# Optimization experiments

Hardware: AMD Instinct MI355X
Metric: run time of the kernel (lower is better)

The kernel has to match this reference:

```python
import jax, jax.numpy as jnp
import numpy as np

P, Q, R = 3, 1, 0          # CliffordAlgebra(p=3, q=1, r=0)
N = P + Q + R
ALG = 1 << N               # 16 basis blades
SHIFTS = (1, 2, 4)


def _cayley():
    """Cayley table C[i,j,k]: blade_i * blade_j = C[i,j,i^j] * blade_{i^j}."""
    metric = [1.0] * P + [-1.0] * Q + [0.0] * R
    C = np.zeros((ALG, ALG, ALG), np.float32)
    for a in range(ALG):
        for b in range(ALG):
            x = a >> 1
            s = 0
            while x:                       # reordering sign
                s += bin(x & b).count('1')
                x >>= 1
            val = -1.0 if (s & 1) else 1.0
            for i in range(N):             # metric for repeated basis vectors
                if (a & b) >> i & 1:
                    val *= metric[i]
            C[a, b, a ^ b] = val
    return C

_C = _cayley()
C0 = jnp.asarray(_C[:, :, 0])                        # grade-0 slice: <a*b>_0
A = jnp.asarray((_C - _C.transpose(1, 0, 2)) / 2.0)  # antisym: (ab - ba)/2
VEC_MASK = jnp.asarray(np.array([1.0 if bin(i).count('1') == 1 else 0.0 for i in range(ALG)], np.float32))
BIV_MASK = jnp.asarray(np.array([1.0 if bin(i).count('1') == 2 else 0.0 for i in range(ALG)], np.float32))


def setup_inputs() -> dict:
    key = jax.random.key(0)
    k1, k2 = jax.random.split(key, 2)
    B, T, D = 8, 4096, 1024
    return {
        "x": jax.random.normal(k1, (B, T, D), jnp.float32),
        "gate_w": jax.random.normal(k2, (D, 1), jnp.float32) * 0.02,
        "gate_b": jnp.zeros((1,), jnp.float32),
        "scalar_weight": jnp.float32(0.5),
        "bivector_weight": jnp.float32(0.5),
    }


def reference(x, gate_w, gate_b, scalar_weight, bivector_weight):
    B, T, D = x.shape
    n = D // ALG                         # 64 chunks of 16 (D divisible, no pad)
    ss = jax.nn.sigmoid(scalar_weight)
    sb = jax.nn.sigmoid(bivector_weight)
    gate = jax.nn.sigmoid(x @ gate_w + gate_b)   # (B,T,1), gate of x (loop-invariant)
    xc = x.reshape(B, T, n, ALG)
    out = x
    for shift in SHIFTS:                 # T=4096 > shift always
        c = x - jnp.roll(x, shift, axis=1)
        cc = c.reshape(B, T, n, ALG)
        # inner product: scalar part per chunk, summed over chunks
        scalar = jnp.einsum('btni,btnj,ij->bt', xc, cc, C0)
        # wedge: antisymmetrized geometric product of vector-grade projections
        av = xc * VEC_MASK
        bv = cc * VEC_MASK
        wedge = jnp.einsum('btni,btnj,ijk->btnk', av, bv, A) * BIV_MASK
        delta = (sb * wedge).reshape(B, T, D)
        delta = delta.at[..., 0].add(ss * scalar)   # scalar_part lives at index 0
        out = out + gate * delta
    return out
```

## Files before the change

kernel.cpp:

```cpp
#include <hip/hip_runtime.h>
#include <math.h>


constexpr int T_DIM = 4096;
constexpr int D_DIM = 1024;
constexpr int ROWS_PER_BLOCK = 4;

__device__ __forceinline__ float sigmoidf(float z) {
    return 1.0f / (1.0f + expf(-z));
}

__global__ __launch_bounds__(256) void clifford_kernel(
    const float* __restrict__ x,
    const float* __restrict__ gate_w,
    const float* __restrict__ gate_b,
    const float* __restrict__ scalar_w,
    const float* __restrict__ bivec_w,
    float* __restrict__ out,
    int BT)
{
    const int lane = threadIdx.x & 63;
    const int row  = blockIdx.x * ROWS_PER_BLOCK + (threadIdx.x >> 6);
    if (row >= BT) return;
    const int b = row >> 12;
    const int t = row & (T_DIM - 1);

    const float ss = sigmoidf(scalar_w[0]);
    const float sb = sigmoidf(bivec_w[0]);
    const float gb = gate_b[0];

    const float* __restrict__ xrow = x + (size_t)row * D_DIM;
    const int base = lane << 4;

    float xa[16], gw[16];
    #pragma unroll
    for (int j = 0; j < 4; ++j) {
        *(float4*)(&xa[4 * j]) = *(const float4*)(xrow + base + 4 * j);
        *(float4*)(&gw[4 * j]) = *(const float4*)(gate_w + base + 4 * j);
    }

    float gate_part = 0.0f;
    #pragma unroll
    for (int i = 0; i < 16; ++i) gate_part += xa[i] * gw[i];

    const float w_blade[16] = { 1.f, 1.f, 1.f,-1.f,  1.f,-1.f,-1.f,-1.f,
                               -1.f, 1.f, 1.f, 1.f,  1.f, 1.f, 1.f,-1.f };

    float sc_part = 0.0f;
    float wacc[6] = {0.f,0.f,0.f,0.f,0.f,0.f};

    #pragma unroll
    for (int si = 0; si < 3; ++si) {
        const int s  = 1 << si;
        const int tp = (t - s) & (T_DIM - 1);
        const float* __restrict__ prow = x + ((size_t)b * T_DIM + tp) * D_DIM;

        float ca[16];
        #pragma unroll
        for (int j = 0; j < 4; ++j) {
            float4 p = *(const float4*)(prow + base + 4 * j);
            ca[4*j+0] = xa[4*j+0] - p.x;
            ca[4*j+1] = xa[4*j+1] - p.y;
            ca[4*j+2] = xa[4*j+2] - p.z;
            ca[4*j+3] = xa[4*j+3] - p.w;
        }

        #pragma unroll
        for (int i = 0; i < 16; ++i) sc_part += w_blade[i] * xa[i] * ca[i];

        wacc[0] += xa[1] * ca[2] - xa[2] * ca[1];
        wacc[1] += xa[1] * ca[4] - xa[4] * ca[1];
        wacc[2] += xa[2] * ca[4] - xa[4] * ca[2];
        wacc[3] += xa[1] * ca[8] - xa[8] * ca[1];
        wacc[4] += xa[2] * ca[8] - xa[8] * ca[2];
        wacc[5] += xa[4] * ca[8] - xa[8] * ca[4];
    }

    #pragma unroll
    for (int off = 32; off > 0; off >>= 1) {
        gate_part += __shfl_xor(gate_part, off, 64);
        sc_part   += __shfl_xor(sc_part,   off, 64);
    }
    const float gate = sigmoidf(gate_part + gb);

    float o[16];
    #pragma unroll
    for (int i = 0; i < 16; ++i) o[i] = xa[i];
    const float gsb = gate * sb;
    o[3]  += gsb * wacc[0];
    o[5]  += gsb * wacc[1];
    o[6]  += gsb * wacc[2];
    o[9]  += gsb * wacc[3];
    o[10] += gsb * wacc[4];
    o[12] += gsb * wacc[5];
    if (lane == 0) o[0] += gate * ss * sc_part;

    float* __restrict__ orow = out + (size_t)row * D_DIM;
    #pragma unroll
    for (int j = 0; j < 4; ++j)
        *(float4*)(orow + base + 4 * j) = *(const float4*)(&o[4 * j]);
}

extern "C" void kernel_launch(void* const* d_in, const int* in_sizes, int n_in,
                              void* d_out, int out_size, void* d_ws, size_t ws_size,
                              hipStream_t stream) {
    const float* x  = (const float*)d_in[0];
    const float* gw = (const float*)d_in[1];
    const float* gb = (const float*)d_in[2];
    const float* sw = (const float*)d_in[3];
    const float* bw = (const float*)d_in[4];
    float* out = (float*)d_out;

    const int BT = in_sizes[0] / D_DIM;
    const int blocks = (BT + ROWS_PER_BLOCK - 1) / ROWS_PER_BLOCK;
    hipLaunchKernelGGL(clifford_kernel, dim3(blocks), dim3(256), 0, stream,
                       x, gw, gb, sw, bw, out, BT);
}
```

Measured before the change: 256.4 us.

## Coalesce loads with 4-lane blade groups, swizzle exchange, and XCD-aware block remap

Each lane now owns 4 contiguous floats per 256-float stride instead of 16 contiguous floats, so wavefront loads are fully coalesced. Wedge terms are gathered across the 4 lanes of a blade chunk with ds_swizzle. The three shift differences are summed algebraically into a single 3x - p1 - p2 - p4, because the inner and wedge products are linear in c. Blocks are remapped so each XCD handles a contiguous range of rows, which should improve L2 reuse of the neighbouring shifted rows. It adds swizzle instructions and per-lane mask arithmetic, and switches to the fast __expf.

```diff
diff --git a/kernel.cpp b/kernel.cpp
--- a/kernel.cpp
+++ b/kernel.cpp
@@ -4,10 +4,18 @@
 
 constexpr int T_DIM = 4096;
 constexpr int D_DIM = 1024;
-constexpr int ROWS_PER_BLOCK = 4;
+
+constexpr int QB0 = 0x8000;
+constexpr int QB1 = 0x8055;
+constexpr int QB2 = 0x80AA;
+
+template <int PAT>
+__device__ __forceinline__ float swz(float v) {
+    return __int_as_float(__builtin_amdgcn_ds_swizzle(__float_as_int(v), PAT));
+}
 
 __device__ __forceinline__ float sigmoidf(float z) {
-    return 1.0f / (1.0f + expf(-z));
+    return 1.0f / (1.0f + __expf(-z));
 }
 
 __global__ __launch_bounds__(256) void clifford_kernel(
@@ -19,86 +27,99 @@
     float* __restrict__ out,
     int BT)
 {
+    int blk = blockIdx.x;
+    if ((gridDim.x & 7) == 0) {
+        const int per = gridDim.x >> 3;
+        blk = (blockIdx.x & 7) * per + (blockIdx.x >> 3);
+    }
+
     const int lane = threadIdx.x & 63;
-    const int row  = blockIdx.x * ROWS_PER_BLOCK + (threadIdx.x >> 6);
+    const int row  = blk * 4 + (threadIdx.x >> 6);
     if (row >= BT) return;
     const int b = row >> 12;
     const int t = row & (T_DIM - 1);
+    const int sub = lane & 3;
 
     const float ss = sigmoidf(scalar_w[0]);
     const float sb = sigmoidf(bivec_w[0]);
     const float gb = gate_b[0];
 
-    const float* __restrict__ xrow = x + (size_t)row * D_DIM;
-    const int base = lane << 4;
+    const float* __restrict__ r0 = x + (size_t)row * D_DIM;
+    const size_t brow = (size_t)b * T_DIM;
+    const float* __restrict__ r1 = x + (brow + ((t - 1) & (T_DIM - 1))) * D_DIM;
+    const float* __restrict__ r2 = x + (brow + ((t - 2) & (T_DIM - 1))) * D_DIM;
+    const float* __restrict__ r4 = x + (brow + ((t - 4) & (T_DIM - 1))) * D_DIM;
 
-    float xa[16], gw[16];
-    #pragma unroll
-    for (int j = 0; j < 4; ++j) {
-        *(float4*)(&xa[4 * j]) = *(const float4*)(xrow + base + 4 * j);
-        *(float4*)(&gw[4 * j]) = *(const float4*)(gate_w + base + 4 * j);
-    }
+    float4 ws;
+    if      (sub == 0) ws = make_float4( 1.f,  1.f,  1.f, -1.f);
+    else if (sub == 1) ws = make_float4( 1.f, -1.f, -1.f, -1.f);
+    else if (sub == 2) ws = make_float4(-1.f,  1.f,  1.f,  1.f);
+    else               ws = make_float4( 1.f,  1.f,  1.f, -1.f);
+    const float m3  = (sub == 0) ? 1.f : 0.f;
+    const float a1  = (sub == 1) ? 1.f : 0.f;
+    const float a2  = (sub == 2) ? 1.f : 0.f;
+    const float m12 = (sub == 3) ? 1.f : 0.f;
 
-    float gate_part = 0.0f;
-    #pragma unroll
-    for (int i = 0; i < 16; ++i) gate_part += xa[i] * gw[i];
-
-    const float w_blade[16] = { 1.f, 1.f, 1.f,-1.f,  1.f,-1.f,-1.f,-1.f,
-                               -1.f, 1.f, 1.f, 1.f,  1.f, 1.f, 1.f,-1.f };
-
-    float sc_part = 0.0f;
-    float wacc[6] = {0.f,0.f,0.f,0.f,0.f,0.f};
+    float4 xs[4], dl[4];
+    float gate_part = 0.f, sc_part = 0.f;
 
     #pragma unroll
-    for (int si = 0; si < 3; ++si) {
-        const int s  = 1 << si;
-        const int tp = (t - s) & (T_DIM - 1);
-        const float* __restrict__ prow = x + ((size_t)b * T_DIM + tp) * D_DIM;
+    for (int m = 0; m < 4; ++m) {
+        const int off = (lane << 2) + (m << 8);
+        const float4 xv = *(const float4*)(r0 + off);
+        const float4 p1 = *(const float4*)(r1 + off);
+        const float4 p2 = *(const float4*)(r2 + off);
+        const float4 p4 = *(const float4*)(r4 + off);
+        const float4 gv = *(const float4*)(gate_w + off);
+        xs[m] = xv;
 
-        float ca[16];
-        #pragma unroll
-        for (int j = 0; j < 4; ++j) {
-            float4 p = *(const float4*)(prow + base + 4 * j);
-            ca[4*j+0] = xa[4*j+0] - p.x;
-            ca[4*j+1] = xa[4*j+1] - p.y;
-            ca[4*j+2] = xa[4*j+2] - p.z;
-            ca[4*j+3] = xa[4*j+3] - p.w;
-        }
+        float4 cs;
+        cs.x = 3.f * xv.x - p1.x - p2.x - p4.x;
+        cs.y = 3.f * xv.y - p1.y - p2.y - p4.y;
+        cs.z = 3.f * xv.z - p1.z - p2.z - p4.z;
+        cs.w = 3.f * xv.w - p1.w - p2.w - p4.w;
 
-        #pragma unroll
-        for (int i = 0; i < 16; ++i) sc_part += w_blade[i] * xa[i] * ca[i];
+        gate_part += xv.x * gv.x + xv.y * gv.y + xv.z * gv.z + xv.w * gv.w;
+        sc_part   += ws.x * (xv.x * cs.x) + ws.y * (xv.y * cs.y)
+                   + ws.z * (xv.z * cs.z) + ws.w * (xv.w * cs.w);
 
-        wacc[0] += xa[1] * ca[2] - xa[2] * ca[1];
-        wacc[1] += xa[1] * ca[4] - xa[4] * ca[1];
-        wacc[2] += xa[2] * ca[4] - xa[4] * ca[2];
-        wacc[3] += xa[1] * ca[8] - xa[8] * ca[1];
-        wacc[4] += xa[2] * ca[8] - xa[8] * ca[2];
-        wacc[5] += xa[4] * ca[8] - xa[8] * ca[4];
+        const float x1 = swz<QB0>(xv.y), x2 = swz<QB0>(xv.z);
+        const float x4b = swz<QB1>(xv.x), x8b = swz<QB2>(xv.x);
+        const float c1 = swz<QB0>(cs.y), c2 = swz<QB0>(cs.z);
+        const float c4b = swz<QB1>(cs.x), c8b = swz<QB2>(cs.x);
+
+        const float w3  = x1 * c2  - x2  * c1;
+        const float w5  = x1 * c4b - x4b * c1;
+        const float w6  = x2 * c4b - x4b * c2;
+        const float w9  = x1 * c8b - x8b * c1;
+        const float w10 = x2 * c8b - x8b * c2;
+        const float w12 = x4b * c8b - x8b * c4b;
+
+        dl[m] = make_float4(m12 * w12,
+                            a1 * w5 + a2 * w9,
+                            a1 * w6 + a2 * w10,
+                            m3 * w3);
     }
 
     #pragma unroll
-    for (int off = 32; off > 0; off >>= 1) {
-        gate_part += __shfl_xor(gate_part, off, 64);
-        sc_part   += __shfl_xor(sc_part,   off, 64);
+    for (int o = 32; o > 0; o >>= 1) {
+        gate_part += __shfl_xor(gate_part, o, 64);
+        sc_part   += __shfl_xor(sc_part,   o, 64);
     }
     const float gate = sigmoidf(gate_part + gb);
-
-    float o[16];
-    #pragma unroll
-    for (int i = 0; i < 16; ++i) o[i] = xa[i];
-    const float gsb = gate * sb;
-    o[3]  += gsb * wacc[0];
-    o[5]  += gsb * wacc[1];
-    o[6]  += gsb * wacc[2];
-    o[9]  += gsb * wacc[3];
-    o[10] += gsb * wacc[4];
-    o[12] += gsb * wacc[5];
-    if (lane == 0) o[0] += gate * ss * sc_part;
+    const float gsb  = gate * sb;
 
     float* __restrict__ orow = out + (size_t)row * D_DIM;
     #pragma unroll
-    for (int j = 0; j < 4; ++j)
-        *(float4*)(orow + base + 4 * j) = *(const float4*)(&o[4 * j]);
+    for (int m = 0; m < 4; ++m) {
+        float4 o4;
+        o4.x = xs[m].x + gsb * dl[m].x;
+        o4.y = xs[m].y + gsb * dl[m].y;
+        o4.z = xs[m].z + gsb * dl[m].z;
+        o4.w = xs[m].w + gsb * dl[m].w;
+        if (m == 0 && lane == 0) o4.x += gate * ss * sc_part;
+        *(float4*)(orow + (lane << 2) + (m << 8)) = o4;
+    }
 }
 
 extern "C" void kernel_launch(void* const* d_in, const int* in_sizes, int n_in,
@@ -112,7 +133,7 @@
     float* out = (float*)d_out;
 
     const int BT = in_sizes[0] / D_DIM;
-    const int blocks = (BT + ROWS_PER_BLOCK - 1) / ROWS_PER_BLOCK;
+    const int blocks = (BT + 3) / 4;
     hipLaunchKernelGGL(clifford_kernel, dim3(blocks), dim3(256), 0, stream,
                        x, gw, gb, sw, bw, out, BT);
 }
```

Result: faster. 244.9 us (-4.5%).
